# Kernel tuning notes

Hardware: AMD Instinct MI355X
Metric: run time of the kernel (lower is better)

Reference implementation:

```python
import jax, jax.numpy as jnp
import numpy as np

N_NODES = 50000
N_EDGES = 600000
ATOM_DIM = 75
HID = 128
N_LAYERS = 4
OUT_DIM = 1
NUM_GRAPHS = 128
EPS = 1e-5


def _bn(x, gamma, beta):
    # BatchNorm1d training-mode forward (biased variance)
    mu = jnp.mean(x, axis=0)
    var = jnp.mean((x - mu) ** 2, axis=0)
    return (x - mu) * jax.lax.rsqrt(var + EPS) * gamma + beta


def setup_inputs() -> dict:
    key = jax.random.key(0)
    ks = jax.random.split(key, 24)
    s = 0.05
    inp = {
        'node_features': jax.random.normal(ks[0], (N_NODES, ATOM_DIM), jnp.float32),
        'edge_index': jax.random.randint(ks[1], (2, N_EDGES), 0, N_NODES, jnp.int32),
        'batch_idx': jnp.sort(jax.random.randint(ks[2], (N_NODES,), 0, NUM_GRAPHS, jnp.int32)),
        # atom embedding: Linear(75->128) + ReLU + BN
        'emb_W': jax.random.normal(ks[3], (HID, ATOM_DIM), jnp.float32) * s,
        'emb_b': jnp.zeros((HID,), jnp.float32),
        'emb_g': jnp.ones((HID,), jnp.float32),
        'emb_beta': jnp.zeros((HID,), jnp.float32),
        # per-layer params, stacked over L=4
        'msg_W': jax.random.normal(ks[4], (N_LAYERS, HID, HID), jnp.float32) * s,
        'msg_b': jnp.zeros((N_LAYERS, HID), jnp.float32),
        'att_W': jax.random.normal(ks[5], (N_LAYERS, 2 * HID), jnp.float32) * s,
        'att_b': jnp.zeros((N_LAYERS,), jnp.float32),
        'gru_Wih': jax.random.normal(ks[6], (N_LAYERS, 3 * HID, HID), jnp.float32) * s,
        'gru_bih': jnp.zeros((N_LAYERS, 3 * HID), jnp.float32),
        'gru_Whh': jax.random.normal(ks[7], (N_LAYERS, 3 * HID, HID), jnp.float32) * s,
        'gru_bhh': jnp.zeros((N_LAYERS, 3 * HID), jnp.float32),
        'bn_g': jnp.ones((N_LAYERS, HID), jnp.float32),
        'bn_b': jnp.zeros((N_LAYERS, HID), jnp.float32),
        # readout: Linear(128->64) + ReLU + Linear(64->1)
        'ro_W1': jax.random.normal(ks[8], (HID // 2, HID), jnp.float32) * s,
        'ro_b1': jnp.zeros((HID // 2,), jnp.float32),
        'ro_W2': jax.random.normal(ks[9], (OUT_DIM, HID // 2), jnp.float32) * s,
        'ro_b2': jnp.zeros((OUT_DIM,), jnp.float32),
    }
    return inp


def _forward(node_features, edge_index, batch_idx, emb_W, emb_b, emb_g, emb_beta,
             msg_W, msg_b, att_W, att_b, gru_Wih, gru_bih, gru_Whh, gru_bhh,
             bn_g, bn_b, ro_W1, ro_b1, ro_W2, ro_b2):
    src, dst = edge_index[0], edge_index[1]
    # atom embedding
    x = _bn(jax.nn.relu(node_features @ emb_W.T + emb_b), emb_g, emb_beta)
    for l in range(N_LAYERS):
        xs = x[src]                                   # [E, h] gather
        xd = x[dst]                                   # [E, h] gather
        ef = jnp.concatenate([xs, xd], axis=1)        # [E, 2h]
        att = jax.nn.sigmoid(ef @ att_W[l] + att_b[l])  # [E]
        msgs = (xs @ msg_W[l].T + msg_b[l]) * att[:, None]  # [E, h]
        agg = jax.ops.segment_sum(msgs, dst, num_segments=N_NODES)  # [N, h]
        # GRUCell(agg, x)
        gi = agg @ gru_Wih[l].T + gru_bih[l]
        gh = x @ gru_Whh[l].T + gru_bhh[l]
        i_r, i_z, i_n = jnp.split(gi, 3, axis=1)
        h_r, h_z, h_n = jnp.split(gh, 3, axis=1)
        r = jax.nn.sigmoid(i_r + h_r)
        z = jax.nn.sigmoid(i_z + h_z)
        n = jnp.tanh(i_n + r * h_n)
        h_new = (1.0 - z) * n + z * x
        x = _bn(h_new, bn_g[l], bn_b[l])              # dropout is identity in eval
    # graph readout: sum-pool per graph
    graph_repr = jax.ops.segment_sum(x, batch_idx, num_segments=NUM_GRAPHS)  # [G, h]
    h1 = jax.nn.relu(graph_repr @ ro_W1.T + ro_b1)
    return h1 @ ro_W2.T + ro_b2                       # [G, 1]


def reference(node_features, edge_index, batch_idx, emb_W, emb_b, emb_g, emb_beta,
              msg_W, msg_b, att_W, att_b, gru_Wih, gru_bih, gru_Whh, gru_bhh,
              bn_g, bn_b, ro_W1, ro_b1, ro_W2, ro_b2):
    return _forward(node_features, edge_index, batch_idx, emb_W, emb_b, emb_g, emb_beta,
                    msg_W, msg_b, att_W, att_b, gru_Wih, gru_bih, gru_Whh, gru_bhh,
                    bn_g, bn_b, ro_W1, ro_b1, ro_W2, ro_b2)
```

## Files before the change

kernel.cpp:

```cpp
#include <hip/hip_runtime.h>
#include <math.h>

#define NN 50000
#define NE 600000
#define ADIM 75
#define HID 128
#define NLAYERS 4
#define NGRAPHS 128
#define BN_EPS 1e-5f
#define NNP 50048
#define NB64 (NNP / 64)

typedef short bhalf8 __attribute__((ext_vector_type(8)));
typedef float floatx4 __attribute__((ext_vector_type(4)));

__device__ __forceinline__ float sigm(float v) { return 1.0f / (1.0f + __expf(-v)); }
__device__ __forceinline__ float tanh_f(float v) {
    return 1.0f - 2.0f / (__expf(2.0f * v) + 1.0f);
}

__device__ __forceinline__ unsigned short f2bf(float f) {
    unsigned u = __builtin_bit_cast(unsigned, f);
    u = (u + 0x7FFFu + ((u >> 16) & 1u)) >> 16;
    return (unsigned short)u;
}
__device__ __forceinline__ float bf2f(unsigned short h) {
    return __builtin_bit_cast(float, ((unsigned)h) << 16);
}

__global__ __launch_bounds__(256) void k_nfb(
    const float* __restrict__ nf, unsigned short* __restrict__ nfb)
{
    int e = blockIdx.x * 256 + threadIdx.x;
    if (e >= NN * 24) return;
    int n = e / 24, k4 = e - n * 24;
    ushort4 o;
    int k = k4 * 4;
    o.x = (k + 0 < ADIM) ? f2bf(nf[(size_t)n * ADIM + k + 0]) : 0;
    o.y = (k + 1 < ADIM) ? f2bf(nf[(size_t)n * ADIM + k + 1]) : 0;
    o.z = (k + 2 < ADIM) ? f2bf(nf[(size_t)n * ADIM + k + 2]) : 0;
    o.w = (k + 3 < ADIM) ? f2bf(nf[(size_t)n * ADIM + k + 3]) : 0;
    ((ushort4*)nfb)[(size_t)n * 24 + k4] = o;
}

__global__ __launch_bounds__(256) void k_wfrag_emb(
    const float* __restrict__ W, unsigned short* __restrict__ web)
{
    int e = blockIdx.x * 256 + threadIdx.x;
    int j = e & 7, n = (e >> 3) & 15, quad = (e >> 7) & 3;
    int kb = (e >> 9) % 3, tc = e / 1536;
    int row = tc * 16 + n;
    int kk = kb * 32 + quad * 8 + j;
    web[e] = (kk < ADIM) ? f2bf(W[row * ADIM + kk]) : 0;
}

__global__ __launch_bounds__(256) void k_embed_m(
    const unsigned short* __restrict__ nfb, const unsigned short* __restrict__ web,
    const float* __restrict__ b, float* __restrict__ y,
    double* __restrict__ bnsum)
{
    __shared__ __align__(16) float hst[64 * 128];
    const int t = threadIdx.x;
    const int wave = t >> 6, lane = t & 63;
    const int col = lane & 15, quad = (lane >> 4) & 3;
    const int node0 = blockIdx.x * 64;

    const int anode = node0 + wave * 16 + col;
    bhalf8 afN[3];
#pragma unroll
    for (int kb = 0; kb < 3; kb++)
        afN[kb] = *(const bhalf8*)&nfb[(size_t)anode * 96 + kb * 32 + quad * 8];

    floatx4 acc[8];
#pragma unroll
    for (int tc = 0; tc < 8; tc++) {
        float bv = b[tc * 16 + col];
        acc[tc] = (floatx4){bv, bv, bv, bv};
    }

#pragma unroll
    for (int tc = 0; tc < 8; tc++) {
        bhalf8 bfr[3];
#pragma unroll
        for (int kb = 0; kb < 3; kb++)
            bfr[kb] = *(const bhalf8*)&web[((tc * 3 + kb) * 64 + lane) * 8];
#pragma unroll
        for (int kb = 0; kb < 3; kb++)
            acc[tc] = __builtin_amdgcn_mfma_f32_16x16x32_bf16(afN[kb], bfr[kb], acc[tc], 0, 0, 0);
    }

#pragma unroll
    for (int tc = 0; tc < 8; tc++)
#pragma unroll
        for (int e = 0; e < 4; e++) {
            float v = fmaxf(acc[tc][e], 0.0f);
            hst[(wave * 16 + quad * 4 + e) * 128 + tc * 16 + col] = v;
        }
    __syncthreads();

#pragma unroll
    for (int i = 0; i < 32; i++) {
        int idx = t + i * 256;
        if (node0 + (idx >> 7) < NN) y[(size_t)node0 * HID + idx] = hst[idx];
    }
    if (t < 128) {
        int count = NN - node0; if (count > 64) count = 64;
        float s = 0.f, s2 = 0.f;
        for (int m = 0; m < count; m++) { float v = hst[m * 128 + t]; s += v; s2 += v * v; }
        unsafeAtomicAdd(&bnsum[t], (double)s);
        unsafeAtomicAdd(&bnsum[128 + t], (double)s2);
    }
}

__global__ __launch_bounds__(256) void k_bnx(
    const float* __restrict__ y, const double* __restrict__ bnsum,
    const float* __restrict__ g, const float* __restrict__ beta,
    const float* __restrict__ attW,
    unsigned short* __restrict__ xb,
    float* __restrict__ as_, float* __restrict__ ad_)
{
    const int t = threadIdx.x;
    const int n = blockIdx.x * 4 + (t >> 6);
    const int lane = t & 63;
    const int f0 = lane * 2;
    double m0 = bnsum[f0] / (double)NN;
    double v0 = bnsum[128 + f0] / (double)NN - m0 * m0;
    double m1 = bnsum[f0 + 1] / (double)NN;
    double v1 = bnsum[128 + f0 + 1] / (double)NN - m1 * m1;
    float sc0 = g[f0] * rsqrtf((float)v0 + BN_EPS);
    float sc1 = g[f0 + 1] * rsqrtf((float)v1 + BN_EPS);
    float sh0 = beta[f0] - (float)m0 * sc0;
    float sh1 = beta[f0 + 1] - (float)m1 * sc1;

    float2 v = ((const float2*)y)[(size_t)n * 64 + lane];
    float2 xv;
    xv.x = v.x * sc0 + sh0;
    xv.y = v.y * sc1 + sh1;
    unsigned pk = (unsigned)f2bf(xv.x) | ((unsigned)f2bf(xv.y) << 16);
    ((unsigned*)xb)[(size_t)n * 64 + lane] = pk;
    float2 aws = ((const float2*)attW)[lane];
    float2 awd = ((const float2*)(attW + 128))[lane];
    float pas = xv.x * aws.x + xv.y * aws.y;
    float pad = xv.x * awd.x + xv.y * awd.y;
#pragma unroll
    for (int msk = 32; msk >= 1; msk >>= 1) {
        pas += __shfl_xor(pas, msk);
        pad += __shfl_xor(pad, msk);
    }
    if (lane == 0) { as_[n] = pas; ad_[n] = pad; }
}

__global__ __launch_bounds__(128) void k_wc(
    const float* __restrict__ Wih, const float* __restrict__ Wm,
    const float* __restrict__ bm, float* __restrict__ Wc, float* __restrict__ bmih)
{
    __shared__ float sw[128];
    __shared__ float red[128];
    const int b = blockIdx.x;
    const int l = b / 384, r = b - l * 384;
    const int t = threadIdx.x;
    const float* wihrow = Wih + ((size_t)l * 384 + r) * 128;
    sw[t] = wihrow[t];
    __syncthreads();
    const float* wm = Wm + (size_t)l * 128 * 128;
    float acc = 0.f;
#pragma unroll 8
    for (int k = 0; k < 128; k++) acc += sw[k] * wm[k * 128 + t];
    Wc[((size_t)l * 384 + r) * 128 + t] = acc;
    red[t] = sw[t] * bm[l * 128 + t];
    __syncthreads();
#pragma unroll
    for (int off = 64; off >= 1; off >>= 1) {
        if (t < off) red[t] += red[t + off];
        __syncthreads();
    }
    if (t == 0) bmih[l * 384 + r] = red[0];
}

__global__ __launch_bounds__(256) void k_frag(
    const float* __restrict__ Wc, const float* __restrict__ Whh,
    unsigned short* __restrict__ wcb, unsigned short* __restrict__ whhb)
{
    const int b = blockIdx.x;
    const int mat = b / 192;
    const int e = (b - mat * 192) * 256 + threadIdx.x;
    const int l = mat >> 1, which = mat & 1;
    const float* src = which ? (Whh + (size_t)l * 49152) : (Wc + (size_t)l * 49152);
    unsigned short* dst = which ? (whhb + (size_t)l * 49152) : (wcb + (size_t)l * 49152);
    int j = e & 7, n = (e >> 3) & 15, quad = (e >> 7) & 3;
    int kb = (e >> 9) & 3, tc = (e >> 11) & 7, g = (e >> 14) & 3;
    int row = g * 128 + tc * 16 + n;
    int kk = kb * 32 + quad * 8 + j;
    dst[e] = f2bf(src[row * 128 + kk]);
}

__global__ __launch_bounds__(256) void k_count(const int* __restrict__ dst, int* __restrict__ cnt)
{
    int e = blockIdx.x * 256 + threadIdx.x;
    if (e < NE) atomicAdd(&cnt[dst[e]], 1);
}

#define SCAN_B 512
#define SCAN_G 98

__global__ __launch_bounds__(SCAN_B) void k_scan1(
    const int* __restrict__ cnt, int* __restrict__ rowptr, int* __restrict__ bsum)
{
    __shared__ int s[SCAN_B];
    const int t = threadIdx.x;
    const int i = blockIdx.x * SCAN_B + t;
    int v = (i < NN) ? cnt[i] : 0;
    s[t] = v;
    __syncthreads();
#pragma unroll
    for (int off = 1; off < SCAN_B; off <<= 1) {
        int u = (t >= off) ? s[t - off] : 0;
        __syncthreads();
        s[t] += u;
        __syncthreads();
    }
    if (i < NN) rowptr[i] = s[t] - v;
    if (t == SCAN_B - 1) bsum[blockIdx.x] = s[t];
}

__global__ __launch_bounds__(128) void k_scan2(int* __restrict__ bsum, int* __restrict__ rowptr)
{
    __shared__ int s[128];
    const int t = threadIdx.x;
    int v = (t < SCAN_G) ? bsum[t] : 0;
    s[t] = v;
    __syncthreads();
#pragma unroll
    for (int off = 1; off < 128; off <<= 1) {
        int u = (t >= off) ? s[t - off] : 0;
        __syncthreads();
        s[t] += u;
        __syncthreads();
    }
    if (t < SCAN_G) bsum[t] = s[t] - v;
    if (t == 127) rowptr[NN] = s[127];
}

__global__ __launch_bounds__(SCAN_B) void k_scan3(
    int* __restrict__ rowptr, const int* __restrict__ bsum, int* __restrict__ wptr)
{
    const int i = blockIdx.x * SCAN_B + threadIdx.x;
    if (i < NN) {
        int v = rowptr[i] + bsum[blockIdx.x];
        rowptr[i] = v;
        wptr[i] = v;
    }
}

__global__ __launch_bounds__(256) void k_scatter(
    const int* __restrict__ src, const int* __restrict__ dst,
    int* __restrict__ wptr, int* __restrict__ ssrc)
{
    int e = blockIdx.x * 256 + threadIdx.x;
    if (e < NE) {
        int d = dst[e];
        int pos = atomicAdd(&wptr[d], 1);
        ssrc[pos] = src[e];
    }
}

__global__ __launch_bounds__(256) void k_gather(
    const int* __restrict__ rowptr, const int* __restrict__ ssrc,
    const unsigned short* __restrict__ xb, const float* __restrict__ as_,
    const float* __restrict__ ad_, const float* __restrict__ attb, int l,
    unsigned short* __restrict__ aggxb, float* __restrict__ sumatt)
{
    const int t = threadIdx.x;
    const int n = blockIdx.x * 8 + (t >> 5);
    const int lane = t & 31;
    const int r0 = rowptr[n], r1 = rowptr[n + 1];
    const float adv = ad_[n] + attb[l];
    float4 acc = make_float4(0.f, 0.f, 0.f, 0.f);
    float satt = 0.f;

    int ids[8], ids2[8];
    if (r0 < r1) {
#pragma unroll
        for (int k = 0; k < 8; k++) {
            int idx = r0 + k; if (idx >= r1) idx = r1 - 1;
            ids[k] = ssrc[idx];
        }
    }
    for (int base = r0; base < r1; base += 8) {
        const int nxt = base + 8;
        if (nxt < r1) {
#pragma unroll
            for (int k = 0; k < 8; k++) {
                int idx = nxt + k; if (idx >= r1) idx = r1 - 1;
                ids2[k] = ssrc[idx];
            }
        }
        ushort4 v[8];
        float a[8];
#pragma unroll
        for (int k = 0; k < 8; k++) {
            v[k] = ((const ushort4*)xb)[(size_t)ids[k] * 32 + lane];
            a[k] = as_[ids[k]];
        }
#pragma unroll
        for (int k = 0; k < 8; k++) {
            if (base + k < r1) {
                float att = sigm(a[k] + adv);
                acc.x += bf2f(v[k].x) * att; acc.y += bf2f(v[k].y) * att;
                acc.z += bf2f(v[k].z) * att; acc.w += bf2f(v[k].w) * att;
                satt += att;
            }
        }
#pragma unroll
        for (int k = 0; k < 8; k++) ids[k] = ids2[k];
    }
    ushort4 o;
    o.x = f2bf(acc.x); o.y = f2bf(acc.y); o.z = f2bf(acc.z); o.w = f2bf(acc.w);
    ((ushort4*)aggxb)[(size_t)n * 32 + lane] = o;
    if (lane == 0) sumatt[n] = satt;
}

#define MMG(AF, ACC, BASE)                                                    \
    _Pragma("unroll")                                                         \
    for (int tc = 0; tc < 8; tc++) {                                          \
        bhalf8 bfr[4];                                                        \
        _Pragma("unroll")                                                     \
        for (int kb = 0; kb < 4; kb++)                                        \
            bfr[kb] = *(const bhalf8*)&(BASE)[((tc * 4 + kb) * 64 + lane) * 8]; \
        _Pragma("unroll")                                                     \
        for (int kb = 0; kb < 4; kb++)                                        \
            ACC[tc] = __builtin_amdgcn_mfma_f32_16x16x32_bf16(AF[kb], bfr[kb], ACC[tc], 0, 0, 0); \
    }

__global__ __launch_bounds__(256) void k_gru(
    const unsigned short* __restrict__ aggxb, const float* __restrict__ sumatt,
    const unsigned short* __restrict__ xb,
    const unsigned short* __restrict__ wcb, const float* __restrict__ bmih,
    const float* __restrict__ bih,
    const unsigned short* __restrict__ whhb, const float* __restrict__ bhh,
    float* __restrict__ y, double* __restrict__ bnsum)
{
    __shared__ __align__(16) float hst[64 * 128];
    const int t = threadIdx.x;
    const int wave = t >> 6, lane = t & 63;
    const int col = lane & 15, quad = (lane >> 4) & 3;
    const int node0 = blockIdx.x * 64;

    const int anode = node0 + wave * 16 + col;
    bhalf8 afA[4], afX[4];
#pragma unroll
    for (int kb = 0; kb < 4; kb++) {
        afA[kb] = *(const bhalf8*)&aggxb[(size_t)anode * HID + kb * 32 + quad * 8];
        afX[kb] = *(const bhalf8*)&xb[(size_t)anode * HID + kb * 32 + quad * 8];
    }
    float sa[4];
#pragma unroll
    for (int e = 0; e < 4; e++) sa[e] = sumatt[node0 + wave * 16 + quad * 4 + e];

    floatx4 accR[8], accN[8];

#pragma unroll
    for (int tc = 0; tc < 8; tc++) {
        int f = 0 * 128 + tc * 16 + col;
        float b0 = bih[f] + bhh[f], bm = bmih[f];
        accR[tc] = (floatx4){b0 + sa[0] * bm, b0 + sa[1] * bm, b0 + sa[2] * bm, b0 + sa[3] * bm};
    }
    MMG(afA, accR, wcb + 0 * 16384);
    MMG(afX, accR, whhb + 0 * 16384);
#pragma unroll
    for (int tc = 0; tc < 8; tc++)
#pragma unroll
        for (int e = 0; e < 4; e++)
            accR[tc][e] = sigm(accR[tc][e]);

#pragma unroll
    for (int tc = 0; tc < 8; tc++) {
        float bh = bhh[2 * 128 + tc * 16 + col];
        accN[tc] = (floatx4){bh, bh, bh, bh};
    }
    MMG(afX, accN, whhb + 2 * 16384);
#pragma unroll
    for (int tc = 0; tc < 8; tc++) {
        int f = 2 * 128 + tc * 16 + col;
        float bi = bih[f], bm = bmih[f];
#pragma unroll
        for (int e = 0; e < 4; e++)
            accN[tc][e] = accR[tc][e] * accN[tc][e] + bi + sa[e] * bm;
    }
    MMG(afA, accN, wcb + 2 * 16384);
#pragma unroll
    for (int tc = 0; tc < 8; tc++)
#pragma unroll
        for (int e = 0; e < 4; e++)
            accN[tc][e] = tanh_f(accN[tc][e]);

#pragma unroll
    for (int tc = 0; tc < 8; tc++) {
        int f = 1 * 128 + tc * 16 + col;
        float b0 = bih[f] + bhh[f], bm = bmih[f];
        accR[tc] = (floatx4){b0 + sa[0] * bm, b0 + sa[1] * bm, b0 + sa[2] * bm, b0 + sa[3] * bm};
    }
    MMG(afA, accR, wcb + 1 * 16384);
    MMG(afX, accR, whhb + 1 * 16384);

#pragma unroll
    for (int tc = 0; tc < 8; tc++) {
#pragma unroll
        for (int e = 0; e < 4; e++) {
            float z = sigm(accR[tc][e]);
            int nd = node0 + wave * 16 + quad * 4 + e;
            float xv = bf2f(xb[(size_t)nd * HID + tc * 16 + col]);
            float h = (1.0f - z) * accN[tc][e] + z * xv;
            hst[(wave * 16 + quad * 4 + e) * 128 + tc * 16 + col] = h;
        }
    }
    __syncthreads();

#pragma unroll
    for (int i = 0; i < 32; i++) {
        int idx = t + i * 256;
        if (node0 + (idx >> 7) < NN) y[(size_t)node0 * HID + idx] = hst[idx];
    }
    if (t < 128) {
        int count = NN - node0; if (count > 64) count = 64;
        float s = 0.f, s2 = 0.f;
        for (int m = 0; m < count; m++) { float v = hst[m * 128 + t]; s += v; s2 += v * v; }
        unsafeAtomicAdd(&bnsum[t], (double)s);
        unsafeAtomicAdd(&bnsum[128 + t], (double)s2);
    }
}

__global__ __launch_bounds__(256) void k_pool(
    const unsigned short* __restrict__ xb, const int* __restrict__ batch,
    float* __restrict__ gr)
{
    __shared__ int sb[256];
    const int t = threadIdx.x;
    const int nb = blockIdx.x * 256;
    int ld = nb + t; if (ld >= NN) ld = NN - 1;
    sb[t] = batch[ld];
    __syncthreads();
    const int s = t >> 7, f = t & 127;
    float acc = 0.f; int cur = -1;
    for (int i = s; i < 256; i += 2) {
        int n = nb + i;
        if (n >= NN) break;
        int g = sb[i];
        if (g != cur) {
            if (cur >= 0) unsafeAtomicAdd(&gr[(size_t)cur * HID + f], acc);
            acc = 0.f; cur = g;
        }
        acc += bf2f(xb[(size_t)n * HID + f]);
    }
    if (cur >= 0) unsafeAtomicAdd(&gr[(size_t)cur * HID + f], acc);
}

__global__ __launch_bounds__(64) void k_readout(
    const float* __restrict__ gr, const float* __restrict__ W1,
    const float* __restrict__ b1, const float* __restrict__ W2,
    const float* __restrict__ b2, float* __restrict__ out)
{
    const int g = blockIdx.x, j = threadIdx.x;
    float acc = b1[j];
    const float4* grow = (const float4*)&gr[g * HID];
    const float4* wrow = (const float4*)&W1[j * HID];
#pragma unroll
    for (int k4 = 0; k4 < 32; k4++) {
        float4 a = grow[k4], w = wrow[k4];
        acc += a.x * w.x + a.y * w.y + a.z * w.z + a.w * w.w;
    }
    float h = fmaxf(acc, 0.0f) * W2[j];
#pragma unroll
    for (int msk = 32; msk >= 1; msk >>= 1) h += __shfl_xor(h, msk);
    if (j == 0) out[g] = h + b2[0];
}

extern "C" void kernel_launch(void* const* d_in, const int* in_sizes, int n_in,
                              void* d_out, int out_size, void* d_ws, size_t ws_size,
                              hipStream_t stream)
{
    const float* nf    = (const float*)d_in[0];
    const int*   ei    = (const int*)d_in[1];
    const int*   batch = (const int*)d_in[2];
    const float* embW  = (const float*)d_in[3];
    const float* embb  = (const float*)d_in[4];
    const float* embg  = (const float*)d_in[5];
    const float* embbe = (const float*)d_in[6];
    const float* msgW  = (const float*)d_in[7];
    const float* msgb  = (const float*)d_in[8];
    const float* attW  = (const float*)d_in[9];
    const float* attb  = (const float*)d_in[10];
    const float* Wih   = (const float*)d_in[11];
    const float* bih   = (const float*)d_in[12];
    const float* Whh   = (const float*)d_in[13];
    const float* bhh   = (const float*)d_in[14];
    const float* bng   = (const float*)d_in[15];
    const float* bnb   = (const float*)d_in[16];
    const float* roW1  = (const float*)d_in[17];
    const float* rob1  = (const float*)d_in[18];
    const float* roW2  = (const float*)d_in[19];
    const float* rob2  = (const float*)d_in[20];
    const int* src = ei;
    const int* dst = ei + NE;
    float* out = (float*)d_out;

    char* base = (char*)d_ws;
    const size_t NH = (size_t)NN * HID;
    double* bnsum = (double*)base;
    float* y     = (float*)(base + 10240);
    unsigned short* xb    = (unsigned short*)(y + NH);
    unsigned short* aggxb = xb + NH;
    float* as_   = (float*)(aggxb + NH);
    float* ad_   = as_ + NN;
    float* sumatt= ad_ + NN;
    float* gr    = sumatt + NN;
    float* Wc    = gr + NGRAPHS * HID;
    float* bmih  = Wc + 4 * 384 * 128;
    int* rowptr  = (int*)(bmih + 4 * 384);
    int* wptr    = rowptr + NN + 4;
    int* cnt     = wptr + NN;
    int* bsum    = cnt + NN;
    int* ssrc    = bsum + 128;
    unsigned short* wcb  = (unsigned short*)(ssrc + NE);
    unsigned short* whhb = wcb + 4 * 49152;
    unsigned short* nfb  = whhb + 4 * 49152;
    unsigned short* web  = nfb + (size_t)NNP * 96;

    k_wc<<<4 * 384, 128, 0, stream>>>(Wih, msgW, msgb, Wc, bmih);
    k_frag<<<8 * 192, 256, 0, stream>>>(Wc, Whh, wcb, whhb);
    k_nfb<<<(NN * 24 + 255) / 256, 256, 0, stream>>>(nf, nfb);
    k_wfrag_emb<<<48, 256, 0, stream>>>(embW, web);
    hipMemsetAsync(cnt, 0, NN * sizeof(int), stream);
    hipMemsetAsync(bnsum, 0, 5 * 256 * sizeof(double), stream);
    k_count<<<(NE + 255) / 256, 256, 0, stream>>>(dst, cnt);
    k_scan1<<<SCAN_G, SCAN_B, 0, stream>>>(cnt, rowptr, bsum);
    k_scan2<<<1, 128, 0, stream>>>(bsum, rowptr);
    k_scan3<<<SCAN_G, SCAN_B, 0, stream>>>(rowptr, bsum, wptr);
    k_scatter<<<(NE + 255) / 256, 256, 0, stream>>>(src, dst, wptr, ssrc);

    k_embed_m<<<NB64, 256, 0, stream>>>(nfb, web, embb, y, bnsum);
    k_bnx<<<NN / 4, 256, 0, stream>>>(y, bnsum, embg, embbe, attW, xb, as_, ad_);

    for (int l = 0; l < NLAYERS; l++) {
        k_gather<<<NN / 8, 256, 0, stream>>>(rowptr, ssrc, xb, as_, ad_, attb, l, aggxb, sumatt);
        k_gru<<<NB64, 256, 0, stream>>>(
            aggxb, sumatt, xb,
            wcb + (size_t)l * 49152, bmih + (size_t)l * 384, bih + (size_t)l * 384,
            whhb + (size_t)l * 49152, bhh + (size_t)l * 384, y, bnsum + (l + 1) * 256);
        const float* attW_next = attW + (size_t)((l + 1 < NLAYERS) ? l + 1 : l) * 256;
        k_bnx<<<NN / 4, 256, 0, stream>>>(y, bnsum + (l + 1) * 256,
                                          bng + (size_t)l * HID, bnb + (size_t)l * HID,
                                          attW_next, xb, as_, ad_);
    }

    hipMemsetAsync(gr, 0, NGRAPHS * HID * sizeof(float), stream);
    k_pool<<<(NN + 255) / 256, 256, 0, stream>>>(xb, batch, gr);
    k_readout<<<NGRAPHS, 64, 0, stream>>>(gr, roW1, rob1, roW2, rob2, out);
}
```

Measured before the change: 697.1 us.

## Stage GRU and embedding weights into LDS with pipelined async loads

Weight fragments for the embedding and GRU matmuls are now copied from global memory into shared memory with global_load_lds. In the GRU they are staged in half-gate chunks through a triple buffer, synchronised with explicit waitcnt and barrier, so the next chunk's load overlaps the current chunk's MFMAs. The goal is to stop each wave re-reading the same weights from global memory and to hide load latency behind compute. In exchange LDS use per block rises (about 80KB for the GRU), which can lower occupancy, and correctness now depends on the hand-written vmcnt counts.

```diff
diff --git a/kernel.cpp b/kernel.cpp
--- a/kernel.cpp
+++ b/kernel.cpp
@@ -26,6 +26,12 @@
 }
 __device__ __forceinline__ float bf2f(unsigned short h) {
     return __builtin_bit_cast(float, ((unsigned)h) << 16);
+}
+
+__device__ __forceinline__ void gl2lds16(const void* g, void* l) {
+    __builtin_amdgcn_global_load_lds(
+        (const __attribute__((address_space(1))) unsigned int*)g,
+        (__attribute__((address_space(3))) unsigned int*)l, 16, 0, 0);
 }
 
 __global__ __launch_bounds__(256) void k_nfb(
@@ -60,11 +66,20 @@
     double* __restrict__ bnsum)
 {
     __shared__ __align__(16) float hst[64 * 128];
+    __shared__ __align__(16) unsigned short wbe[12288];
     const int t = threadIdx.x;
     const int wave = t >> 6, lane = t & 63;
     const int col = lane & 15, quad = (lane >> 4) & 3;
     const int node0 = blockIdx.x * 64;
 
+    {
+        const char* gsrc = (const char*)web + wave * 6144 + lane * 16;
+        char* ldst = (char*)wbe + wave * 6144;
+#pragma unroll
+        for (int i = 0; i < 6; i++)
+            gl2lds16(gsrc + i * 1024, ldst + i * 1024);
+    }
+
     const int anode = node0 + wave * 16 + col;
     bhalf8 afN[3];
 #pragma unroll
@@ -77,13 +92,14 @@
         float bv = b[tc * 16 + col];
         acc[tc] = (floatx4){bv, bv, bv, bv};
     }
+    __syncthreads();
 
 #pragma unroll
     for (int tc = 0; tc < 8; tc++) {
         bhalf8 bfr[3];
 #pragma unroll
         for (int kb = 0; kb < 3; kb++)
-            bfr[kb] = *(const bhalf8*)&web[((tc * 3 + kb) * 64 + lane) * 8];
+            bfr[kb] = *(const bhalf8*)&wbe[((tc * 3 + kb) * 64 + lane) * 8];
 #pragma unroll
         for (int kb = 0; kb < 3; kb++)
             acc[tc] = __builtin_amdgcn_mfma_f32_16x16x32_bf16(afN[kb], bfr[kb], acc[tc], 0, 0, 0);
@@ -320,17 +336,30 @@
     if (lane == 0) sumatt[n] = satt;
 }
 
-#define MMG(AF, ACC, BASE)                                                    \
+#define STAGE_H(SRC, DST)                                                     \
+    {                                                                         \
+        const char* gsrc_ = (const char*)(SRC) + wave * 4096 + lane * 16;     \
+        char* ldst_ = (char*)(DST) + wave * 4096;                             \
+        _Pragma("unroll")                                                     \
+        for (int i_ = 0; i_ < 4; i_++)                                        \
+            gl2lds16(gsrc_ + i_ * 1024, ldst_ + i_ * 1024);                   \
+    }
+
+#define MMGL_H(AF, ACC, TCOFF, BUF)                                           \
     _Pragma("unroll")                                                         \
-    for (int tc = 0; tc < 8; tc++) {                                          \
+    for (int tc = 0; tc < 4; tc++) {                                          \
         bhalf8 bfr[4];                                                        \
         _Pragma("unroll")                                                     \
         for (int kb = 0; kb < 4; kb++)                                        \
-            bfr[kb] = *(const bhalf8*)&(BASE)[((tc * 4 + kb) * 64 + lane) * 8]; \
+            bfr[kb] = *(const bhalf8*)&(BUF)[((tc * 4 + kb) * 64 + lane) * 8];\
         _Pragma("unroll")                                                     \
         for (int kb = 0; kb < 4; kb++)                                        \
-            ACC[tc] = __builtin_amdgcn_mfma_f32_16x16x32_bf16(AF[kb], bfr[kb], ACC[tc], 0, 0, 0); \
-    }
+            (ACC)[(TCOFF) + tc] = __builtin_amdgcn_mfma_f32_16x16x32_bf16(    \
+                AF[kb], bfr[kb], (ACC)[(TCOFF) + tc], 0, 0, 0);               \
+    }
+
+#define WBAR4() asm volatile("s_waitcnt vmcnt(4)\n\ts_barrier" ::: "memory")
+#define WBAR0() asm volatile("s_waitcnt vmcnt(0)\n\ts_barrier" ::: "memory")
 
 __global__ __launch_bounds__(256) void k_gru(
     const unsigned short* __restrict__ aggxb, const float* __restrict__ sumatt,
@@ -341,10 +370,23 @@
     float* __restrict__ y, double* __restrict__ bnsum)
 {
     __shared__ __align__(16) float hst[64 * 128];
+    __shared__ __align__(16) unsigned short wbuf[3][8192];
     const int t = threadIdx.x;
     const int wave = t >> 6, lane = t & 63;
     const int col = lane & 15, quad = (lane >> 4) & 3;
     const int node0 = blockIdx.x * 64;
+
+    const unsigned short* const sch[12] = {
+        wcb,          wcb + 8192,
+        whhb,         whhb + 8192,
+        whhb + 32768, whhb + 40960,
+        wcb + 32768,  wcb + 40960,
+        wcb + 16384,  wcb + 24576,
+        whhb + 16384, whhb + 24576
+    };
+
+    STAGE_H(sch[0], wbuf[0]);
+    STAGE_H(sch[1], wbuf[1]);
 
     const int anode = node0 + wave * 16 + col;
     bhalf8 afA[4], afX[4];
@@ -365,43 +407,68 @@
         float b0 = bih[f] + bhh[f], bm = bmih[f];
         accR[tc] = (floatx4){b0 + sa[0] * bm, b0 + sa[1] * bm, b0 + sa[2] * bm, b0 + sa[3] * bm};
     }
-    MMG(afA, accR, wcb + 0 * 16384);
-    MMG(afX, accR, whhb + 0 * 16384);
-#pragma unroll
-    for (int tc = 0; tc < 8; tc++)
-#pragma unroll
-        for (int e = 0; e < 4; e++)
-            accR[tc][e] = sigm(accR[tc][e]);
-
+
+    WBAR4(); STAGE_H(sch[2], wbuf[2]); MMGL_H(afA, accR, 0, wbuf[0]);
+    WBAR4(); STAGE_H(sch[3], wbuf[0]); MMGL_H(afA, accR, 4, wbuf[1]);
+    WBAR4(); STAGE_H(sch[4], wbuf[1]); MMGL_H(afX, accR, 0, wbuf[2]);
+#pragma unroll
+    for (int tc = 0; tc < 4; tc++)
+#pragma unroll
+        for (int e = 0; e < 4; e++) accR[tc][e] = sigm(accR[tc][e]);
+
+    WBAR4(); STAGE_H(sch[5], wbuf[2]); MMGL_H(afX, accR, 4, wbuf[0]);
+#pragma unroll
+    for (int tc = 4; tc < 8; tc++)
+#pragma unroll
+        for (int e = 0; e < 4; e++) accR[tc][e] = sigm(accR[tc][e]);
 #pragma unroll
     for (int tc = 0; tc < 8; tc++) {
         float bh = bhh[2 * 128 + tc * 16 + col];
         accN[tc] = (floatx4){bh, bh, bh, bh};
     }
-    MMG(afX, accN, whhb + 2 * 16384);
-#pragma unroll
-    for (int tc = 0; tc < 8; tc++) {
+
+    WBAR4(); STAGE_H(sch[6], wbuf[0]); MMGL_H(afX, accN, 0, wbuf[1]);
+#pragma unroll
+    for (int tc = 0; tc < 4; tc++) {
         int f = 2 * 128 + tc * 16 + col;
         float bi = bih[f], bm = bmih[f];
 #pragma unroll
         for (int e = 0; e < 4; e++)
             accN[tc][e] = accR[tc][e] * accN[tc][e] + bi + sa[e] * bm;
     }
-    MMG(afA, accN, wcb + 2 * 16384);
-#pragma unroll
-    for (int tc = 0; tc < 8; tc++)
+
+    WBAR4(); STAGE_H(sch[7], wbuf[1]); MMGL_H(afX, accN, 4, wbuf[2]);
+#pragma unroll
+    for (int tc = 4; tc < 8; tc++) {
+        int f = 2 * 128 + tc * 16 + col;
+        float bi = bih[f], bm = bmih[f];
 #pragma unroll
         for (int e = 0; e < 4; e++)
-            accN[tc][e] = tanh_f(accN[tc][e]);
-
+            accN[tc][e] = accR[tc][e] * accN[tc][e] + bi + sa[e] * bm;
+    }
 #pragma unroll
     for (int tc = 0; tc < 8; tc++) {
         int f = 1 * 128 + tc * 16 + col;
         float b0 = bih[f] + bhh[f], bm = bmih[f];
         accR[tc] = (floatx4){b0 + sa[0] * bm, b0 + sa[1] * bm, b0 + sa[2] * bm, b0 + sa[3] * bm};
     }
-    MMG(afA, accR, wcb + 1 * 16384);
-    MMG(afX, accR, whhb + 1 * 16384);
+
+    WBAR4(); STAGE_H(sch[8], wbuf[2]); MMGL_H(afA, accN, 0, wbuf[0]);
+#pragma unroll
+    for (int tc = 0; tc < 4; tc++)
+#pragma unroll
+        for (int e = 0; e < 4; e++) accN[tc][e] = tanh_f(accN[tc][e]);
+
+    WBAR4(); STAGE_H(sch[9], wbuf[0]); MMGL_H(afA, accN, 4, wbuf[1]);
+#pragma unroll
+    for (int tc = 4; tc < 8; tc++)
+#pragma unroll
+        for (int e = 0; e < 4; e++) accN[tc][e] = tanh_f(accN[tc][e]);
+
+    WBAR4(); STAGE_H(sch[10], wbuf[1]); MMGL_H(afA, accR, 0, wbuf[2]);
+    WBAR4(); STAGE_H(sch[11], wbuf[2]); MMGL_H(afA, accR, 4, wbuf[0]);
+    WBAR4();                            MMGL_H(afX, accR, 0, wbuf[1]);
+    WBAR0();                            MMGL_H(afX, accR, 4, wbuf[2]);
 
 #pragma unroll
     for (int tc = 0; tc < 8; tc++) {
```

New measurement: 648.5 us. 1.07x faster.
